# Kernel tuning notes

Hardware: AMD Instinct MI355X
Metric: run time of the kernel (lower is better)

## Reference

```python
import jax, jax.numpy as jnp
import numpy as np

EMBEDDING_DIM = 64
N_EMBEDDINGS = 512


def setup_inputs() -> dict:
    key = jax.random.key(0)
    k1, k2 = jax.random.split(key)
    inputs = jax.random.normal(k1, (32, 64, 64, 64), dtype=jnp.float32)  # NCHW, C==embedding_dim
    weight = jax.random.normal(k2, (N_EMBEDDINGS, EMBEDDING_DIM), dtype=jnp.float32)
    return {"inputs": inputs, "weight": weight}


def reference(inputs, weight):
    # NCHW -> NHWC, flatten to [N, D]
    x = jnp.transpose(inputs, (0, 2, 3, 1))  # [B, H, W, D]
    in_shape = x.shape
    flat = x.reshape(-1, EMBEDDING_DIM)  # [N, D]

    distances = (
        jnp.sum(flat * flat, axis=1, keepdims=True)
        + jnp.sum(weight * weight, axis=1)
        - 2.0 * flat @ weight.T
    )
    idx = jnp.argmin(distances, axis=1)  # [N]

    # one-hot @ weight is just a gather
    quantized = weight[idx].reshape(in_shape)  # [B, H, W, D]

    # commitment loss: mse(stop_grad(quantized), x)
    e_latent_loss = jnp.mean(jnp.square(jax.lax.stop_gradient(quantized) - x))

    # straight-through estimator
    quantized = x + jax.lax.stop_gradient(quantized - x)

    return jnp.transpose(quantized, (0, 3, 1, 2)), e_latent_loss
```

## Files before the change

kernel.cpp:

```cpp
#include <hip/hip_runtime.h>
#include <math.h>

typedef short bf16x8 __attribute__((ext_vector_type(8)));
typedef float f32x4 __attribute__((ext_vector_type(4)));

#define VQ_D 64
#define VQ_K 512
#define VQ_NQ 131072
#define VQ_TOTAL 8388608
#define QB 256
#define NT 32
#define XPITCH 136

__device__ __forceinline__ ushort bf16_rne(float f) {
    uint u = __builtin_bit_cast(uint, f);
    u += 0x7fffu + ((u >> 16) & 1u);
    return (ushort)(u >> 16);
}
__device__ __forceinline__ float bf16_to_f(ushort h) {
    uint u = ((uint)h) << 16;
    return __builtin_bit_cast(float, u);
}

__global__ __launch_bounds__(128) void vq_prep(const float* __restrict__ w,
                                               ushort* __restrict__ wfrag,
                                               float* __restrict__ wn,
                                               float* __restrict__ out) {
    if (blockIdx.x == 0 && threadIdx.x == 0) out[VQ_TOTAL] = 0.f;
    const int k = blockIdx.x * 128 + threadIdx.x;
    const float4* row = (const float4*)(w + k * VQ_D);
    const int t = k >> 4, col = k & 15;
    float nrm = 0.f;
    for (int g = 0; g < 8; ++g) {
        float4 a = row[2 * g], b4 = row[2 * g + 1];
        float v[8] = {a.x, a.y, a.z, a.w, b4.x, b4.y, b4.z, b4.w};
        ushort hi[8], lo[8];
#pragma unroll
        for (int j = 0; j < 8; ++j) {
            nrm = fmaf(v[j], v[j], nrm);
            hi[j] = bf16_rne(v[j]);
            lo[j] = bf16_rne(v[j] - bf16_to_f(hi[j]));
        }
        const int quad = g & 3, fh = g >> 2;
        const int lane = quad * 16 + col;
        bf16x8* basez = (bf16x8*)wfrag + t * 256 + lane;
        *(basez + fh * 64)       = *(bf16x8*)hi;
        *(basez + (2 + fh) * 64) = *(bf16x8*)lo;
    }
    wn[k] = nrm;
}

__global__ __launch_bounds__(256, 2) void vq_main(const float* __restrict__ in,
                                                  const float* __restrict__ w,
                                                  const ushort* __restrict__ wfrag,
                                                  const float* __restrict__ wng,
                                                  float* __restrict__ out) {
    __shared__ ushort x_lds[128 * XPITCH];
    __shared__ float wn_lds[VQ_K];
    __shared__ float xn_lds[2][QB];
    __shared__ float best_lds[QB], sec_lds[QB];
    __shared__ int   bi_lds[QB], si_lds[QB];

    const int tid  = threadIdx.x;
    const int lane = tid & 63;
    const int wid  = tid >> 6;
    const int col  = lane & 15;
    const int quad = lane >> 4;
    const int n0  = blockIdx.x * QB;
    const int b   = n0 >> 12;
    const int hw0 = n0 & 4095;
    const float* xg = in + (b << 18) + hw0;

    wn_lds[tid]       = wng[tid];
    wn_lds[tid + 256] = wng[tid + 256];

    bf16x8 ah0[4], ah1[4], al0[4], al1[4];
    const int q_l = tid & 127, gh = tid >> 7;
    const int arow_l = (wid & 1) * 64 + col;

#pragma unroll
    for (int p = 0; p < 2; ++p) {
        {
            const float* xq = xg + p * 128 + q_l;
            float xnp = 0.f;
#pragma unroll
            for (int i = 0; i < 4; ++i) {
                const int g = gh * 4 + i;
                float v[8];
                ushort hi[8], lo[8];
#pragma unroll
                for (int j = 0; j < 8; ++j) v[j] = xq[(g * 8 + j) << 12];
#pragma unroll
                for (int j = 0; j < 8; ++j) {
                    xnp = fmaf(v[j], v[j], xnp);
                    hi[j] = bf16_rne(v[j]);
                    lo[j] = bf16_rne(v[j] - bf16_to_f(hi[j]));
                }
                *(bf16x8*)&x_lds[q_l * XPITCH + g * 8]      = *(bf16x8*)hi;
                *(bf16x8*)&x_lds[q_l * XPITCH + 64 + g * 8] = *(bf16x8*)lo;
            }
            xn_lds[gh][p * 128 + q_l] = xnp;
        }
        __syncthreads();
        if ((wid >> 1) == p) {
#pragma unroll
            for (int T = 0; T < 4; ++T) {
                const ushort* xr = x_lds + (arow_l + T * 16) * XPITCH;
                ah0[T] = *(const bf16x8*)(xr + quad * 8);
                ah1[T] = *(const bf16x8*)(xr + 32 + quad * 8);
                al0[T] = *(const bf16x8*)(xr + 64 + quad * 8);
                al1[T] = *(const bf16x8*)(xr + 96 + quad * 8);
            }
        }
        __syncthreads();
    }

    float best[16], secnd[16];
#pragma unroll
    for (int r = 0; r < 16; ++r) { best[r] = 3.0e38f; secnd[r] = 3.0e38f; }

    const bf16x8* wf = (const bf16x8*)wfrag + lane;
    bf16x8 bh0 = wf[0], bh1 = wf[64], bl0 = wf[128], bl1 = wf[192];

    for (int t = 0; t < NT; ++t) {
        bf16x8 nh0, nh1, nl0, nl1;
        if (t + 1 < NT) {
            const bf16x8* nx = wf + (t + 1) * 256;
            nh0 = nx[0]; nh1 = nx[64]; nl0 = nx[128]; nl1 = nx[192];
        }
        const float wnv = wn_lds[t * 16 + col];
#pragma unroll
        for (int T = 0; T < 4; ++T) {
            f32x4 accP = {0.f, 0.f, 0.f, 0.f}, accQ = {0.f, 0.f, 0.f, 0.f};
            accP = __builtin_amdgcn_mfma_f32_16x16x32_bf16(ah0[T], bh0, accP, 0, 0, 0);
            accP = __builtin_amdgcn_mfma_f32_16x16x32_bf16(ah1[T], bh1, accP, 0, 0, 0);
            accQ = __builtin_amdgcn_mfma_f32_16x16x32_bf16(ah0[T], bl0, accQ, 0, 0, 0);
            accQ = __builtin_amdgcn_mfma_f32_16x16x32_bf16(ah1[T], bl1, accQ, 0, 0, 0);
            accQ = __builtin_amdgcn_mfma_f32_16x16x32_bf16(al0[T], bh0, accQ, 0, 0, 0);
            accQ = __builtin_amdgcn_mfma_f32_16x16x32_bf16(al1[T], bh1, accQ, 0, 0, 0);
#pragma unroll
            for (int j = 0; j < 4; ++j) {
                float dist = fmaf(-2.f, accP[j] + accQ[j], wnv);
                uint u = (__builtin_bit_cast(uint, dist) & 0xFFFFFFE0u) | (uint)t;
                float key = __builtin_bit_cast(float, u);
                const int r = T * 4 + j;
                float m = fmaxf(best[r], key);
                best[r]  = fminf(best[r], key);
                secnd[r] = fminf(secnd[r], m);
            }
        }
        bh0 = nh0; bh1 = nh1; bl0 = nl0; bl1 = nl1;
    }

    float bD[16], sD[16];
    int bI[16], sI[16];
#pragma unroll
    for (int r = 0; r < 16; ++r) {
        uint ub = __builtin_bit_cast(uint, best[r]);
        uint us = __builtin_bit_cast(uint, secnd[r]);
        bI[r] = (int)(ub & 31u) * 16 + col;
        sI[r] = (int)(us & 31u) * 16 + col;
        bD[r] = __builtin_bit_cast(float, ub & 0xFFFFFFE0u);
        sD[r] = __builtin_bit_cast(float, us & 0xFFFFFFE0u);
    }

#pragma unroll
    for (int off = 1; off < 16; off <<= 1) {
#pragma unroll
        for (int r = 0; r < 16; ++r) {
            float ob = __shfl_xor(bD[r], off, 64);
            float os = __shfl_xor(sD[r], off, 64);
            int   oi = __shfl_xor(bI[r], off, 64);
            int   oc = __shfl_xor(sI[r], off, 64);
            bool oWins = (ob < bD[r]) || (ob == bD[r] && oi < bI[r]);
            float nb  = oWins ? ob    : bD[r];
            int   ni  = oWins ? oi    : bI[r];
            float c1  = oWins ? bD[r] : ob;
            int   ci1 = oWins ? bI[r] : oi;
            float c2  = oWins ? os    : sD[r];
            int   ci2 = oWins ? oc    : sI[r];
            bool c1w = (c1 < c2) || (c1 == c2 && ci1 < ci2);
            sD[r] = c1w ? c1  : c2;
            sI[r] = c1w ? ci1 : ci2;
            bD[r] = nb; bI[r] = ni;
        }
    }
    if (col == 0) {
#pragma unroll
        for (int r = 0; r < 16; ++r) {
            const int q = wid * 64 + (r >> 2) * 16 + quad * 4 + (r & 3);
            best_lds[q] = bD[r]; sec_lds[q] = sD[r];
            bi_lds[q] = bI[r];   si_lds[q] = sI[r];
        }
    }
    __syncthreads();

    {
        const int q = tid;
        float cb = best_lds[q], cs = sec_lds[q];
        int cbi = bi_lds[q], csi = si_lds[q];
        double chosen = (double)cb;
        if (cs - cb < 8e-3f) {
            const float* wb  = w + cbi * VQ_D;
            const float* ws2 = w + csi * VQ_D;
            const float* xqp = xg + q;
            double nb = 0.0, dotb = 0.0, ns = 0.0, dots = 0.0;
            for (int d = 0; d < VQ_D; ++d) {
                double xv = (double)xqp[d << 12];
                double wbv = (double)wb[d], wsv = (double)ws2[d];
                nb = fma(wbv, wbv, nb); dotb = fma(xv, wbv, dotb);
                ns = fma(wsv, wsv, ns); dots = fma(xv, wsv, dots);
            }
            double db = nb - 2.0 * dotb, ds = ns - 2.0 * dots;
            if (ds < db || (ds == db && csi < cbi)) { cbi = csi; chosen = ds; }
            else                                    { chosen = db; }
        }
        bi_lds[q] = cbi;
        double lq = (double)(xn_lds[0][q] + xn_lds[1][q]) + chosen;
#pragma unroll
        for (int off = 32; off > 0; off >>= 1)
            lq += __shfl_down(lq, off, 64);
        if ((tid & 63) == 0)
            atomicAdd(out + VQ_TOTAL, (float)(lq * (1.0 / (double)VQ_TOTAL)));
    }
    __syncthreads();

    {
        const int q = tid;
        const float4* wrow = (const float4*)(w + bi_lds[q] * VQ_D);
        float* op = out + (b << 18) + hw0 + q;
#pragma unroll
        for (int i = 0; i < 16; ++i) {
            float4 v = wrow[i];
            op[(4 * i + 0) << 12] = v.x;
            op[(4 * i + 1) << 12] = v.y;
            op[(4 * i + 2) << 12] = v.z;
            op[(4 * i + 3) << 12] = v.w;
        }
    }
}

extern "C" void kernel_launch(void* const* d_in, const int* in_sizes, int n_in,
                              void* d_out, int out_size, void* d_ws, size_t ws_size,
                              hipStream_t stream) {
    const float* in = (const float*)d_in[0];
    const float* w  = (const float*)d_in[1];
    float* out = (float*)d_out;

    ushort* wfrag = (ushort*)d_ws;
    float*  wn    = (float*)((char*)d_ws + 131072);

    vq_prep<<<4, 128, 0, stream>>>(w, wfrag, wn, out);
    vq_main<<<VQ_NQ / QB, 256, 0, stream>>>(in, w, wfrag, wn, out);
}
```

Baseline: 141.9 us.

## Halve queries per block, load A fragments directly from global, drop LDS staging

Each block now handles 128 queries instead of 256, and each wave owns 32 queries. Waves build their bf16 hi/lo A fragments straight from global memory into registers, with no LDS transpose staging or the barriers it needed. Codebook norms are read from global with prefetch rather than staged in LDS, and occupancy is raised to 3 blocks per SM. This doubles the grid and halves reuse of each codebook fragment load per query, and the direct global loads may coalesce less well.

```diff
diff --git a/kernel.cpp b/kernel.cpp
--- a/kernel.cpp
+++ b/kernel.cpp
@@ -8,9 +8,8 @@
 #define VQ_K 512
 #define VQ_NQ 131072
 #define VQ_TOTAL 8388608
-#define QB 256
 #define NT 32
-#define XPITCH 136
+#define TAU 8e-3f
 
 __device__ __forceinline__ ushort bf16_rne(float f) {
     uint u = __builtin_bit_cast(uint, f);
@@ -50,87 +49,67 @@
     wn[k] = nrm;
 }
 
-__global__ __launch_bounds__(256, 2) void vq_main(const float* __restrict__ in,
+__global__ __launch_bounds__(256, 3) void vq_main(const float* __restrict__ in,
                                                   const float* __restrict__ w,
                                                   const ushort* __restrict__ wfrag,
                                                   const float* __restrict__ wng,
                                                   float* __restrict__ out) {
-    __shared__ ushort x_lds[128 * XPITCH];
-    __shared__ float wn_lds[VQ_K];
-    __shared__ float xn_lds[2][QB];
-    __shared__ float best_lds[QB], sec_lds[QB];
-    __shared__ int   bi_lds[QB], si_lds[QB];
+    __shared__ float xn_lds[128];
+    __shared__ float best_lds[128], sec_lds[128];
+    __shared__ int   bi_lds[128], si_lds[128];
 
     const int tid  = threadIdx.x;
     const int lane = tid & 63;
     const int wid  = tid >> 6;
     const int col  = lane & 15;
     const int quad = lane >> 4;
-    const int n0  = blockIdx.x * QB;
+    const int n0  = blockIdx.x * 128;
     const int b   = n0 >> 12;
     const int hw0 = n0 & 4095;
-    const float* xg = in + (b << 18) + hw0;
-
-    wn_lds[tid]       = wng[tid];
-    wn_lds[tid + 256] = wng[tid + 256];
-
-    bf16x8 ah0[4], ah1[4], al0[4], al1[4];
-    const int q_l = tid & 127, gh = tid >> 7;
-    const int arow_l = (wid & 1) * 64 + col;
-
-#pragma unroll
-    for (int p = 0; p < 2; ++p) {
-        {
-            const float* xq = xg + p * 128 + q_l;
-            float xnp = 0.f;
-#pragma unroll
-            for (int i = 0; i < 4; ++i) {
-                const int g = gh * 4 + i;
-                float v[8];
-                ushort hi[8], lo[8];
-#pragma unroll
-                for (int j = 0; j < 8; ++j) v[j] = xq[(g * 8 + j) << 12];
-#pragma unroll
-                for (int j = 0; j < 8; ++j) {
-                    xnp = fmaf(v[j], v[j], xnp);
-                    hi[j] = bf16_rne(v[j]);
-                    lo[j] = bf16_rne(v[j] - bf16_to_f(hi[j]));
-                }
-                *(bf16x8*)&x_lds[q_l * XPITCH + g * 8]      = *(bf16x8*)hi;
-                *(bf16x8*)&x_lds[q_l * XPITCH + 64 + g * 8] = *(bf16x8*)lo;
-            }
-            xn_lds[gh][p * 128 + q_l] = xnp;
-        }
-        __syncthreads();
-        if ((wid >> 1) == p) {
-#pragma unroll
-            for (int T = 0; T < 4; ++T) {
-                const ushort* xr = x_lds + (arow_l + T * 16) * XPITCH;
-                ah0[T] = *(const bf16x8*)(xr + quad * 8);
-                ah1[T] = *(const bf16x8*)(xr + 32 + quad * 8);
-                al0[T] = *(const bf16x8*)(xr + 64 + quad * 8);
-                al1[T] = *(const bf16x8*)(xr + 96 + quad * 8);
-            }
-        }
-        __syncthreads();
-    }
-
-    float best[16], secnd[16];
-#pragma unroll
-    for (int r = 0; r < 16; ++r) { best[r] = 3.0e38f; secnd[r] = 3.0e38f; }
+    const float* xg0 = in + (b << 18) + hw0;
+    const float* xgW = xg0 + wid * 32;
+
+    bf16x8 ah0[2], ah1[2], al0[2], al1[2];
+#pragma unroll
+    for (int T = 0; T < 2; ++T) {
+        const float* xq = xgW + T * 16 + col;
+        float sx = 0.f;
+        ushort h0[8], l0[8], h1[8], l1[8];
+#pragma unroll
+        for (int j = 0; j < 8; ++j) {
+            float v0 = xq[(quad * 8 + j) << 12];
+            float v1 = xq[(32 + quad * 8 + j) << 12];
+            sx = fmaf(v0, v0, sx);
+            sx = fmaf(v1, v1, sx);
+            h0[j] = bf16_rne(v0); l0[j] = bf16_rne(v0 - bf16_to_f(h0[j]));
+            h1[j] = bf16_rne(v1); l1[j] = bf16_rne(v1 - bf16_to_f(h1[j]));
+        }
+        ah0[T] = *(bf16x8*)h0; al0[T] = *(bf16x8*)l0;
+        ah1[T] = *(bf16x8*)h1; al1[T] = *(bf16x8*)l1;
+        sx += __shfl_xor(sx, 16, 64);
+        sx += __shfl_xor(sx, 32, 64);
+        if (quad == 0) xn_lds[wid * 32 + T * 16 + col] = sx;
+    }
+
+    float best[8], sec[8];
+#pragma unroll
+    for (int r = 0; r < 8; ++r) { best[r] = 3.0e38f; sec[r] = 3.0e38f; }
 
     const bf16x8* wf = (const bf16x8*)wfrag + lane;
     bf16x8 bh0 = wf[0], bh1 = wf[64], bl0 = wf[128], bl1 = wf[192];
-
+    float wnv = wng[col];
+
+#pragma unroll 1
     for (int t = 0; t < NT; ++t) {
         bf16x8 nh0, nh1, nl0, nl1;
+        float wnn;
         if (t + 1 < NT) {
             const bf16x8* nx = wf + (t + 1) * 256;
             nh0 = nx[0]; nh1 = nx[64]; nl0 = nx[128]; nl1 = nx[192];
-        }
-        const float wnv = wn_lds[t * 16 + col];
-#pragma unroll
-        for (int T = 0; T < 4; ++T) {
+            wnn = wng[(t + 1) * 16 + col];
+        }
+#pragma unroll
+        for (int T = 0; T < 2; ++T) {
             f32x4 accP = {0.f, 0.f, 0.f, 0.f}, accQ = {0.f, 0.f, 0.f, 0.f};
             accP = __builtin_amdgcn_mfma_f32_16x16x32_bf16(ah0[T], bh0, accP, 0, 0, 0);
             accP = __builtin_amdgcn_mfma_f32_16x16x32_bf16(ah1[T], bh1, accP, 0, 0, 0);
@@ -145,19 +124,19 @@
                 float key = __builtin_bit_cast(float, u);
                 const int r = T * 4 + j;
                 float m = fmaxf(best[r], key);
-                best[r]  = fminf(best[r], key);
-                secnd[r] = fminf(secnd[r], m);
+                best[r] = fminf(best[r], key);
+                sec[r]  = fminf(sec[r], m);
             }
         }
-        bh0 = nh0; bh1 = nh1; bl0 = nl0; bl1 = nl1;
-    }
-
-    float bD[16], sD[16];
-    int bI[16], sI[16];
-#pragma unroll
-    for (int r = 0; r < 16; ++r) {
+        bh0 = nh0; bh1 = nh1; bl0 = nl0; bl1 = nl1; wnv = wnn;
+    }
+
+    float bD[8], sD[8];
+    int bI[8], sI[8];
+#pragma unroll
+    for (int r = 0; r < 8; ++r) {
         uint ub = __builtin_bit_cast(uint, best[r]);
-        uint us = __builtin_bit_cast(uint, secnd[r]);
+        uint us = __builtin_bit_cast(uint, sec[r]);
         bI[r] = (int)(ub & 31u) * 16 + col;
         sI[r] = (int)(us & 31u) * 16 + col;
         bD[r] = __builtin_bit_cast(float, ub & 0xFFFFFFE0u);
@@ -167,7 +146,7 @@
 #pragma unroll
     for (int off = 1; off < 16; off <<= 1) {
 #pragma unroll
-        for (int r = 0; r < 16; ++r) {
+        for (int r = 0; r < 8; ++r) {
             float ob = __shfl_xor(bD[r], off, 64);
             float os = __shfl_xor(sD[r], off, 64);
             int   oi = __shfl_xor(bI[r], off, 64);
@@ -187,23 +166,23 @@
     }
     if (col == 0) {
 #pragma unroll
-        for (int r = 0; r < 16; ++r) {
-            const int q = wid * 64 + (r >> 2) * 16 + quad * 4 + (r & 3);
+        for (int r = 0; r < 8; ++r) {
+            const int q = wid * 32 + (r >> 2) * 16 + quad * 4 + (r & 3);
             best_lds[q] = bD[r]; sec_lds[q] = sD[r];
             bi_lds[q] = bI[r];   si_lds[q] = sI[r];
         }
     }
     __syncthreads();
 
-    {
+    if (tid < 128) {
         const int q = tid;
         float cb = best_lds[q], cs = sec_lds[q];
         int cbi = bi_lds[q], csi = si_lds[q];
         double chosen = (double)cb;
-        if (cs - cb < 8e-3f) {
+        if (cs - cb < TAU) {
             const float* wb  = w + cbi * VQ_D;
             const float* ws2 = w + csi * VQ_D;
-            const float* xqp = xg + q;
+            const float* xqp = xg0 + q;
             double nb = 0.0, dotb = 0.0, ns = 0.0, dots = 0.0;
             for (int d = 0; d < VQ_D; ++d) {
                 double xv = (double)xqp[d << 12];
@@ -216,7 +195,7 @@
             else                                    { chosen = db; }
         }
         bi_lds[q] = cbi;
-        double lq = (double)(xn_lds[0][q] + xn_lds[1][q]) + chosen;
+        double lq = (double)xn_lds[q] + chosen;
 #pragma unroll
         for (int off = 32; off > 0; off >>= 1)
             lq += __shfl_down(lq, off, 64);
@@ -226,16 +205,17 @@
     __syncthreads();
 
     {
-        const int q = tid;
-        const float4* wrow = (const float4*)(w + bi_lds[q] * VQ_D);
+        const int q = tid & 127, half = tid >> 7;
+        const float4* wrow = (const float4*)(w + bi_lds[q] * VQ_D) + half * 8;
         float* op = out + (b << 18) + hw0 + q;
 #pragma unroll
-        for (int i = 0; i < 16; ++i) {
-            float4 v = wrow[i];
-            op[(4 * i + 0) << 12] = v.x;
-            op[(4 * i + 1) << 12] = v.y;
-            op[(4 * i + 2) << 12] = v.z;
-            op[(4 * i + 3) << 12] = v.w;
+        for (int u = 0; u < 8; ++u) {
+            float4 v = wrow[u];
+            const int d = half * 32 + 4 * u;
+            op[(d + 0) << 12] = v.x;
+            op[(d + 1) << 12] = v.y;
+            op[(d + 2) << 12] = v.z;
+            op[(d + 3) << 12] = v.w;
         }
     }
 }
@@ -251,5 +231,5 @@
     float*  wn    = (float*)((char*)d_ws + 131072);
 
     vq_prep<<<4, 128, 0, stream>>>(w, wfrag, wn, out);
-    vq_main<<<VQ_NQ / QB, 256, 0, stream>>>(in, w, wfrag, wn, out);
-}
+    vq_main<<<VQ_NQ / 128, 256, 0, stream>>>(in, w, wfrag, wn, out);
+}
```

Result: no change. 139.7 us (-1.5%).
